# Kernel optimization log

Hardware: AMD Instinct MI355X
Metric: run time of the kernel (lower is better)

## Reference

```python
import jax, jax.numpy as jnp
import numpy as np

TOP_K = 30
NUM_RBF = 16
NUM_POS = 16
MAX_REL = 32
EDGE_FEATURES = 128
EDGE_IN = NUM_POS + NUM_RBF * 9 + 7  # 167


def _normalize(x, axis=-1):
    # torch F.normalize: x / max(||x||, 1e-12)
    return x / jnp.maximum(jnp.linalg.norm(x, axis=axis, keepdims=True), 1e-12)


def _gather_nodes(nodes, idx):
    # nodes [B,L,C], idx [B,L,K] -> [B,L,K,C]
    return jax.vmap(lambda n, i: n[i])(nodes, idx)


def _rbf(D):
    D_mu = jnp.linspace(2.0, 22.0, NUM_RBF)  # [R]
    D_sigma = (22.0 - 2.0) / NUM_RBF
    return jnp.exp(-(((D[..., None] - D_mu) / D_sigma) ** 2))


def _get_rbf(A, B, E_idx):
    # full pairwise dist then gather neighbors (faithful to source)
    D_A_B = jnp.sqrt(jnp.sum((A[:, :, None, :] - B[:, None, :, :]) ** 2, -1) + 1e-6)
    D_nb = jnp.take_along_axis(D_A_B, E_idx, axis=2)  # [B,L,K]
    return _rbf(D_nb)


def _quaternions(R):
    # R [B,L,K,3,3] -> Q [B,L,K,4]
    diag = jnp.diagonal(R, axis1=-2, axis2=-1)  # [B,L,K,3]
    Rxx, Ryy, Rzz = diag[..., 0], diag[..., 1], diag[..., 2]
    magnitudes = 0.5 * jnp.sqrt(jnp.abs(1 + jnp.stack(
        [Rxx - Ryy - Rzz, -Rxx + Ryy - Rzz, -Rxx - Ryy + Rzz], -1)))
    signs = jnp.sign(jnp.stack([
        R[..., 2, 1] - R[..., 1, 2],
        R[..., 0, 2] - R[..., 2, 0],
        R[..., 1, 0] - R[..., 0, 1]], -1))
    xyz = signs * magnitudes
    w = jnp.sqrt(jax.nn.relu(1 + jnp.sum(diag, -1, keepdims=True))) / 2.0
    return _normalize(jnp.concatenate((xyz, w), -1))


def _orientations_coarse(X, E_idx, eps=1e-6):
    B, L, _ = X.shape
    dX = X[:, 1:, :] - X[:, :-1, :]
    dX_norm = jnp.linalg.norm(dX, axis=-1)
    dX_mask = (dX_norm > 3.6) & (dX_norm < 4.0)
    dX = dX * dX_mask[:, :, None]
    U = _normalize(dX)
    u_2, u_1, u_0 = U[:, :-2, :], U[:, 1:-1, :], U[:, 2:, :]
    n_2 = _normalize(jnp.cross(u_2, u_1))
    o_1 = _normalize(u_2 - u_1)
    # local frames O [B,L-3,3,3] -> flattened, padded to [B,L,9]
    O = jnp.stack((o_1, n_2, jnp.cross(o_1, n_2)), 2).reshape(B, L - 3, 9)
    O = jnp.pad(O, ((0, 0), (1, 2), (0, 0)))
    O_neighbors = _gather_nodes(O, E_idx)        # [B,L,K,9]
    X_neighbors = _gather_nodes(X, E_idx)        # [B,L,K,3]
    O = O.reshape(B, L, 3, 3)
    O_neighbors = O_neighbors.reshape(*E_idx.shape, 3, 3)
    dXn = X_neighbors - X[:, :, None, :]
    dU = _normalize(jnp.einsum('blij,blkj->blki', O, dXn))
    R = jnp.einsum('blji,blkjm->blkim', O, O_neighbors)  # O^T @ O_nb
    Q = _quaternions(R)
    return jnp.concatenate((dU, Q), -1)  # [B,L,K,7]


def setup_inputs() -> dict:
    B, L = 2, 4096
    key = jax.random.key(0)
    ks = jax.random.split(key, 6)
    Ca = jax.random.normal(ks[0], (B, L, 3), dtype=jnp.float32)
    mask = jnp.ones((B, L), dtype=jnp.float32)
    residue_idx = jnp.arange(B * L, dtype=jnp.int32).reshape(B, L)
    chain_labels = jnp.sort(jax.random.randint(ks[1], (B, L), 0, 4), axis=-1).astype(jnp.int32)
    pos_in = 2 * MAX_REL + 1 + 1  # 66
    pos_W = jax.random.normal(ks[2], (NUM_POS, pos_in), dtype=jnp.float32) / np.sqrt(pos_in)
    pos_b = jnp.zeros((NUM_POS,), dtype=jnp.float32)
    edge_W = jax.random.normal(ks[3], (EDGE_FEATURES, EDGE_IN), dtype=jnp.float32) / np.sqrt(EDGE_IN)
    ln_g = jnp.ones((EDGE_FEATURES,), dtype=jnp.float32)
    ln_b = jnp.zeros((EDGE_FEATURES,), dtype=jnp.float32)
    return {"Ca": Ca, "mask": mask, "residue_idx": residue_idx,
            "chain_labels": chain_labels, "pos_W": pos_W, "pos_b": pos_b,
            "edge_W": edge_W, "ln_g": ln_g, "ln_b": ln_b}


def _forward(Ca, mask, residue_idx, chain_labels, pos_W, pos_b, edge_W, ln_g, ln_b):
    B, L, _ = Ca.shape
    # _dist: masked pairwise distances + kNN
    mask_2D = mask[:, :, None] * mask[:, None, :]
    dX = Ca[:, None, :, :] - Ca[:, :, None, :]
    D = mask_2D * jnp.sqrt(jnp.sum(dX ** 2, 3) + 1e-6)
    D_max = jnp.max(D, -1, keepdims=True)
    D_adjust = D + (1.0 - mask_2D) * D_max
    k = min(TOP_K, L)
    neg_vals, E_idx = jax.lax.top_k(-D_adjust, k)  # smallest-k
    D_neighbors = -neg_vals

    zeros = jnp.zeros((B, 1, 3), dtype=Ca.dtype)
    Ca_0 = jnp.concatenate([zeros, Ca[:, :-1, :]], axis=1)
    Ca_1 = Ca
    Ca_2 = jnp.concatenate([Ca[:, 1:, :], zeros], axis=1)

    O_features = _orientations_coarse(Ca, E_idx)

    RBF_all = jnp.concatenate([
        _rbf(D_neighbors),
        _get_rbf(Ca_0, Ca_0, E_idx), _get_rbf(Ca_2, Ca_2, E_idx),
        _get_rbf(Ca_0, Ca_1, E_idx), _get_rbf(Ca_0, Ca_2, E_idx),
        _get_rbf(Ca_1, Ca_0, E_idx), _get_rbf(Ca_1, Ca_2, E_idx),
        _get_rbf(Ca_2, Ca_0, E_idx), _get_rbf(Ca_2, Ca_1, E_idx)], axis=-1)

    offset = residue_idx[:, :, None] - residue_idx[:, None, :]
    offset = jnp.take_along_axis(offset, E_idx, axis=2)  # [B,L,K]
    d_chains = (chain_labels[:, :, None] - chain_labels[:, None, :] == 0).astype(jnp.int32)
    E_chains = jnp.take_along_axis(d_chains, E_idx, axis=2)

    # PositionalEncodings
    d = jnp.clip(offset + MAX_REL, 0, 2 * MAX_REL) * E_chains + (1 - E_chains) * (2 * MAX_REL + 1)
    d_onehot = jax.nn.one_hot(d, 2 * MAX_REL + 2, dtype=jnp.float32)
    E_positional = d_onehot @ pos_W.T + pos_b

    E = jnp.concatenate((E_positional, RBF_all, O_features), -1)  # [B,L,K,167]
    E = E @ edge_W.T
    mu = jnp.mean(E, -1, keepdims=True)
    var = jnp.var(E, -1, keepdims=True)
    E = (E - mu) / jnp.sqrt(var + 1e-5) * ln_g + ln_b
    return E, E_idx


def reference(Ca, mask, residue_idx, chain_labels, pos_W, pos_b, edge_W, ln_g, ln_b):
    return _forward(Ca, mask, residue_idx, chain_labels, pos_W, pos_b, edge_W, ln_g, ln_b)
```

## Files before the change

kernel.cpp:

```cpp
#include <hip/hip_runtime.h>
#include <stdint.h>

#define LL 4096
#define NB 2
#define KK 30
#define CDIM 128
#define FROW 200

typedef _Float16 half_t;
typedef half_t half8 __attribute__((ext_vector_type(8)));
typedef float f32x4 __attribute__((ext_vector_type(4)));

__device__ __forceinline__ float3 loadCa(const float* __restrict__ Ca, int b, int idx) {
    const float* p = Ca + ((size_t)(b * LL + idx)) * 3;
    return make_float3(p[0], p[1], p[2]);
}
__device__ __forceinline__ float3 shiftedCa(const float* __restrict__ Ca, int b, int idx, int sel) {
    int jj = idx + sel - 1;
    if (jj < 0 || jj >= LL) return make_float3(0.f, 0.f, 0.f);
    return loadCa(Ca, b, jj);
}
__device__ __forceinline__ float sgnf(float x) { return (x > 0.f) ? 1.f : ((x < 0.f) ? -1.f : 0.f); }
__device__ __forceinline__ float pdist(float3 a, float3 c) {
    float dx = a.x - c.x, dy = a.y - c.y, dz = a.z - c.z;
    return sqrtf(dx * dx + dy * dy + dz * dz + 1e-6f);
}

__global__ __launch_bounds__(256) void prep_kernel(const float* __restrict__ W,
                                                   const float* __restrict__ posW,
                                                   const float* __restrict__ posb,
                                                   const float* __restrict__ Ca,
                                                   half_t* __restrict__ Bp,
                                                   half_t* __restrict__ pwt,
                                                   float* __restrict__ Of) {
    int blk = blockIdx.x;
    int tid = threadIdx.x;
    if (blk < 12) {
        int idx = blk * 256 + tid;
        if (idx >= 8 * 6 * 64) return;
        int l = idx & 63;
        int ts = idx >> 6;
        int s = ts % 6, t = ts / 6;
        int n = 16 * t + (l & 15);
        int kbase = 32 * s + 8 * (l >> 4);
        half8 v;
#pragma unroll
        for (int e = 0; e < 8; e++) {
            int k = kbase + e;
            v[e] = (k < 167) ? (half_t)W[n * 167 + k] : (half_t)0.f;
        }
        *(half8*)(Bp + (size_t)idx * 8) = v;
    } else if (blk < 17) {
        int idx = (blk - 12) * 256 + tid;
        if (idx < 66 * 16) {
            int d = idx >> 4, p = idx & 15;
            pwt[d * 16 + p] = (half_t)(posW[p * 66 + d] + posb[p]);
        }
    } else {
        int t = (blk - 17) * 256 + tid;
        if (t >= NB * LL) return;
        int b = t >> 12, i = t & (LL - 1);
        float o[9] = {0.f, 0.f, 0.f, 0.f, 0.f, 0.f, 0.f, 0.f, 0.f};
        if (i >= 1 && i <= LL - 3) {
            float3 cm = loadCa(Ca, b, i - 1), cc = loadCa(Ca, b, i), cp = loadCa(Ca, b, i + 1);
            float dx0 = cc.x - cm.x, dy0 = cc.y - cm.y, dz0 = cc.z - cm.z;
            float n0 = sqrtf(dx0 * dx0 + dy0 * dy0 + dz0 * dz0);
            float k0 = (n0 > 3.6f && n0 < 4.0f) ? 1.f : 0.f;
            float s0 = k0 / fmaxf(n0 * k0, 1e-12f);
            float u2x = dx0 * s0, u2y = dy0 * s0, u2z = dz0 * s0;
            float dx1 = cp.x - cc.x, dy1 = cp.y - cc.y, dz1 = cp.z - cc.z;
            float n1 = sqrtf(dx1 * dx1 + dy1 * dy1 + dz1 * dz1);
            float k1 = (n1 > 3.6f && n1 < 4.0f) ? 1.f : 0.f;
            float s1 = k1 / fmaxf(n1 * k1, 1e-12f);
            float u1x = dx1 * s1, u1y = dy1 * s1, u1z = dz1 * s1;
            float cx = u2y * u1z - u2z * u1y;
            float cy = u2z * u1x - u2x * u1z;
            float cz = u2x * u1y - u2y * u1x;
            float cn = sqrtf(cx * cx + cy * cy + cz * cz);
            float cinv = 1.f / fmaxf(cn, 1e-12f);
            float n2x = cx * cinv, n2y = cy * cinv, n2z = cz * cinv;
            float ox = u2x - u1x, oy = u2y - u1y, oz = u2z - u1z;
            float on = sqrtf(ox * ox + oy * oy + oz * oz);
            float oinv = 1.f / fmaxf(on, 1e-12f);
            float o1x = ox * oinv, o1y = oy * oinv, o1z = oz * oinv;
            o[0] = o1x; o[1] = o1y; o[2] = o1z;
            o[3] = n2x; o[4] = n2y; o[5] = n2z;
            o[6] = o1y * n2z - o1z * n2y;
            o[7] = o1z * n2x - o1x * n2z;
            o[8] = o1x * n2y - o1y * n2x;
        }
        float* dst = Of + (size_t)t * 9;
#pragma unroll
        for (int r = 0; r < 9; r++) dst[r] = o[r];
    }
}

__global__ __launch_bounds__(256, 8) void topk_kernel(const float* __restrict__ Ca,
                                                      const float* __restrict__ mask,
                                                      int* __restrict__ eidx_ws,
                                                      float* __restrict__ dnb_ws,
                                                      float* __restrict__ out_eidx_f) {
    __shared__ unsigned long long cand[512];
    __shared__ int wint[2][4];
    __shared__ int gcnt[4];
    __shared__ float wflt[4];
    int row = blockIdx.x;
    int b = row >> 12;
    int tid = threadIdx.x;
    int w = tid >> 6, lane = tid & 63;
    float3 ci = loadCa(Ca, b, row & (LL - 1));
    float mi = mask[row];
    float dreg[16];
    float localmax = 0.f;
#pragma unroll
    for (int s = 0; s < 16; s++) {
        int j = tid + s * 256;
        const float* pj = Ca + ((size_t)(b * LL + j)) * 3;
        float dx = pj[0] - ci.x, dy = pj[1] - ci.y, dz = pj[2] - ci.z;
        float d = sqrtf(dx * dx + dy * dy + dz * dz + 1e-6f);
        float D = mi * mask[b * LL + j] * d;
        dreg[s] = D;
        localmax = fmaxf(localmax, D);
    }
#pragma unroll
    for (int o = 32; o; o >>= 1) localmax = fmaxf(localmax, __shfl_xor(localmax, o));
    if (lane == 0) wflt[w] = localmax;
    __syncthreads();
    float dmax = fmaxf(fmaxf(wflt[0], wflt[1]), fmaxf(wflt[2], wflt[3]));
    unsigned ui[16];
#pragma unroll
    for (int s = 0; s < 16; s++) {
        int j = tid + s * 256;
        float m2 = mi * mask[b * LL + j];
        ui[s] = __float_as_uint(dreg[s] + (1.0f - m2) * dmax);
    }
    unsigned lo = 0u, hi = 0x7f800000u, T = 0u;
    bool found = false;
    int p = 0;
    for (int it = 0; it < 24 && !found; ++it) {
        unsigned mid = (lo + hi) >> 1;
        int c = 0;
#pragma unroll
        for (int s = 0; s < 16; s++) c += (ui[s] < mid) ? 1 : 0;
#pragma unroll
        for (int o = 32; o; o >>= 1) c += __shfl_xor(c, o);
        if (lane == 0) wint[p][w] = c;
        __syncthreads();
        c = wint[p][0] + wint[p][1] + wint[p][2] + wint[p][3];
        p ^= 1;
        if (c < 30) lo = mid;
        else if (c > 64) hi = mid;
        else { T = mid; found = true; }
    }
    if (!found) T = hi;
    int cnt = 0;
#pragma unroll
    for (int s = 0; s < 16; s++) cnt += (ui[s] < T) ? 1 : 0;
    int inc = cnt;
#pragma unroll
    for (int o = 1; o < 64; o <<= 1) {
        int nv = __shfl_up(inc, o);
        if (lane >= o) inc += nv;
    }
    if (lane == 63) gcnt[w] = inc;
    __syncthreads();
    int C = gcnt[0] + gcnt[1] + gcnt[2] + gcnt[3];
    int waveoff = 0;
    for (int q = 0; q < 4; q++) waveoff += (q < w) ? gcnt[q] : 0;
    int slot = waveoff + inc - cnt;
#pragma unroll
    for (int s = 0; s < 16; s++) {
        if (ui[s] < T) {
            int j = tid + s * 256;
            if (slot < 512)
                cand[slot] = ((unsigned long long)ui[s] << 32) | (unsigned)j;
            slot++;
        }
    }
    __syncthreads();
    if (w != 0) return;
    if (C <= 64) {
        unsigned long long v = (lane < C) ? cand[lane] : ~0ull;
#pragma unroll
        for (int k = 2; k <= 64; k <<= 1) {
#pragma unroll
            for (int jj = k >> 1; jj > 0; jj >>= 1) {
                unsigned long long o = __shfl_xor(v, jj);
                bool take_min = (((lane & jj) == 0) == ((lane & k) == 0));
                bool lt = (o < v);
                v = (take_min == lt) ? o : v;
            }
        }
        if (lane < KK) {
            int j = (int)(v & 0xffffffffu);
            eidx_ws[row * KK + lane] = j;
            dnb_ws[row * KK + lane] = __uint_as_float((unsigned)(v >> 32));
            out_eidx_f[row * KK + lane] = (float)j;
        }
    } else {
        unsigned long long r[8];
#pragma unroll
        for (int q = 0; q < 8; q++) {
            int idx = lane + 64 * q;
            r[q] = (idx < C && idx < 512) ? cand[idx] : ~0ull;
        }
        for (int t = 0; t < KK; t++) {
            unsigned long long v = r[0];
#pragma unroll
            for (int q = 1; q < 8; q++) v = (r[q] < v) ? r[q] : v;
#pragma unroll
            for (int o = 32; o; o >>= 1) {
                unsigned long long u = __shfl_xor(v, o);
                if (u < v) v = u;
            }
            if (lane == 0) {
                int j = (int)(v & 0xffffffffu);
                eidx_ws[row * KK + t] = j;
                dnb_ws[row * KK + t] = __uint_as_float((unsigned)(v >> 32));
                out_eidx_f[row * KK + t] = (float)j;
            }
#pragma unroll
            for (int q = 0; q < 8; q++)
                if (r[q] == v) r[q] = ~0ull;
        }
    }
}

__global__ __launch_bounds__(256) void edge_kernel(const float* __restrict__ Ca,
                                                   const int* __restrict__ ridx,
                                                   const int* __restrict__ chl,
                                                   const half_t* __restrict__ pwt,
                                                   const half_t* __restrict__ Bp,
                                                   const float* __restrict__ ln_g,
                                                   const float* __restrict__ ln_b,
                                                   const float* __restrict__ Of,
                                                   const int* __restrict__ eidx_ws,
                                                   const float* __restrict__ dnb_ws,
                                                   float* __restrict__ outE) {
    __shared__ alignas(16) half_t featH[64][FROW];
    __shared__ float sD[60][10];
    __shared__ float psum[64][4];
    __shared__ float pssq[64][4];
    __shared__ float rmu[64], rinv[64];
    int row0 = blockIdx.x * 2;
    int b = row0 >> 12;
    int tid = threadIdx.x;

    if (tid < 120) {
        int e = tid >> 1, half = tid & 1;
        int isr1 = (e >= KK) ? 1 : 0;
        int grow = row0 + isr1;
        int ke = e - (isr1 ? KK : 0);
        int i = grow & (LL - 1);
        int j = eidx_ws[grow * KK + ke];
        if (half == 0) {
            float3 Pi0 = shiftedCa(Ca, b, i, 0);
            float3 Pi2 = shiftedCa(Ca, b, i, 2);
            float3 Pj0 = shiftedCa(Ca, b, j, 0);
            float3 Pj1 = loadCa(Ca, b, j);
            float3 Pj2 = shiftedCa(Ca, b, j, 2);
            sD[e][0] = dnb_ws[grow * KK + ke];
            sD[e][1] = pdist(Pi0, Pj0);
            sD[e][2] = pdist(Pi2, Pj2);
            sD[e][3] = pdist(Pi0, Pj1);
            sD[e][4] = pdist(Pi0, Pj2);
            int off = ridx[grow] - ridx[b * LL + j];
            int eqc = (chl[grow] == chl[b * LL + j]) ? 1 : 0;
            int d = off + 32;
            d = d < 0 ? 0 : (d > 64 ? 64 : d);
            d = eqc ? d : 65;
            *(half8*)&featH[e][0] = *(const half8*)(pwt + d * 16);
            *(half8*)&featH[e][8] = *(const half8*)(pwt + d * 16 + 8);
        } else {
            float3 Pi1 = loadCa(Ca, b, i);
            float3 Pi2 = shiftedCa(Ca, b, i, 2);
            float3 Pj0 = shiftedCa(Ca, b, j, 0);
            float3 Pj1 = loadCa(Ca, b, j);
            float3 Pj2 = shiftedCa(Ca, b, j, 2);
            sD[e][5] = pdist(Pi1, Pj0);
            sD[e][6] = pdist(Pi1, Pj2);
            sD[e][7] = pdist(Pi2, Pj0);
            sD[e][8] = pdist(Pi2, Pj1);
            float Oi[9], Oj[9];
#pragma unroll
            for (int r = 0; r < 9; r++) {
                Oi[r] = Of[(size_t)grow * 9 + r];
                Oj[r] = Of[((size_t)(b * LL + j)) * 9 + r];
            }
            float dx = Pj1.x - Pi1.x, dy = Pj1.y - Pi1.y, dz = Pj1.z - Pi1.z;
            float v0 = Oi[0] * dx + Oi[1] * dy + Oi[2] * dz;
            float v1 = Oi[3] * dx + Oi[4] * dy + Oi[5] * dz;
            float v2 = Oi[6] * dx + Oi[7] * dy + Oi[8] * dz;
            float nn = sqrtf(v0 * v0 + v1 * v1 + v2 * v2);
            float ninv = 1.f / fmaxf(nn, 1e-12f);
            float R[3][3];
#pragma unroll
            for (int m = 0; m < 3; m++)
#pragma unroll
                for (int n = 0; n < 3; n++)
                    R[m][n] = Oi[0 * 3 + m] * Oj[0 * 3 + n] + Oi[1 * 3 + m] * Oj[1 * 3 + n] +
                              Oi[2 * 3 + m] * Oj[2 * 3 + n];
            float Rxx = R[0][0], Ryy = R[1][1], Rzz = R[2][2];
            float m0 = 0.5f * sqrtf(fabsf(1.f + Rxx - Ryy - Rzz));
            float m1 = 0.5f * sqrtf(fabsf(1.f - Rxx + Ryy - Rzz));
            float m2 = 0.5f * sqrtf(fabsf(1.f - Rxx - Ryy + Rzz));
            float x = sgnf(R[2][1] - R[1][2]) * m0;
            float y = sgnf(R[0][2] - R[2][0]) * m1;
            float z = sgnf(R[1][0] - R[0][1]) * m2;
            float ww = 0.5f * sqrtf(fmaxf(1.f + Rxx + Ryy + Rzz, 0.f));
            float qn = sqrtf(x * x + y * y + z * z + ww * ww);
            float qi = 1.f / fmaxf(qn, 1e-12f);
            half8 h;
            h[0] = (half_t)(v0 * ninv);
            h[1] = (half_t)(v1 * ninv);
            h[2] = (half_t)(v2 * ninv);
            h[3] = (half_t)(x * qi);
            h[4] = (half_t)(y * qi);
            h[5] = (half_t)(z * qi);
            h[6] = (half_t)(ww * qi);
            h[7] = (half_t)0.f;
            half8 zv = {};
            *(half8*)&featH[e][160] = h;
            *(half8*)&featH[e][168] = zv;
            *(half8*)&featH[e][176] = zv;
            *(half8*)&featH[e][184] = zv;
        }
    } else if (tid >= 156) {
        int t = tid - 156;
        int r = 60 + t / 25, c = t % 25;
        half8 zv = {};
        *(half8*)&featH[r][c * 8] = zv;
    }
    __syncthreads();

    for (int job = tid; job < 540; job += 256) {
        int e = job / 9, q = job - e * 9;
        float D = sD[e][q];
        half8 v0, v1;
#pragma unroll
        for (int m = 0; m < 8; m++) {
            float mu = 2.0f + (4.f / 3.f) * (float)m;
            float t = (D - mu) * 0.8f;
            v0[m] = (half_t)exp2f(t * t * -1.4426950408889634f);
        }
#pragma unroll
        for (int m = 8; m < 16; m++) {
            float mu = 2.0f + (4.f / 3.f) * (float)m;
            float t = (D - mu) * 0.8f;
            v1[m - 8] = (half_t)exp2f(t * t * -1.4426950408889634f);
        }
        *(half8*)&featH[e][16 + 16 * q] = v0;
        *(half8*)&featH[e][24 + 16 * q] = v1;
    }
    __syncthreads();

    int lane = tid & 63, w = tid >> 6;
    int cc = lane & 15, g = lane >> 4;
    f32x4 zero = {0.f, 0.f, 0.f, 0.f};
    f32x4 acc[4][2];
#pragma unroll
    for (int m = 0; m < 4; m++) {
        acc[m][0] = zero;
        acc[m][1] = zero;
    }
    const half_t* b0p = Bp + ((size_t)(2 * w) * 6) * 64 * 8;
    const half_t* b1p = Bp + ((size_t)(2 * w + 1) * 6) * 64 * 8;
    for (int s = 0; s < 6; s++) {
        int ko = 32 * s + 8 * g;
        half8 af0 = *(const half8*)&featH[cc][ko];
        half8 af1 = *(const half8*)&featH[16 + cc][ko];
        half8 af2 = *(const half8*)&featH[32 + cc][ko];
        half8 af3 = *(const half8*)&featH[48 + cc][ko];
        half8 bf0 = *(const half8*)(b0p + (size_t)(s * 64 + lane) * 8);
        half8 bf1 = *(const half8*)(b1p + (size_t)(s * 64 + lane) * 8);
        acc[0][0] = __builtin_amdgcn_mfma_f32_16x16x32_f16(af0, bf0, acc[0][0], 0, 0, 0);
        acc[0][1] = __builtin_amdgcn_mfma_f32_16x16x32_f16(af0, bf1, acc[0][1], 0, 0, 0);
        acc[1][0] = __builtin_amdgcn_mfma_f32_16x16x32_f16(af1, bf0, acc[1][0], 0, 0, 0);
        acc[1][1] = __builtin_amdgcn_mfma_f32_16x16x32_f16(af1, bf1, acc[1][1], 0, 0, 0);
        acc[2][0] = __builtin_amdgcn_mfma_f32_16x16x32_f16(af2, bf0, acc[2][0], 0, 0, 0);
        acc[2][1] = __builtin_amdgcn_mfma_f32_16x16x32_f16(af2, bf1, acc[2][1], 0, 0, 0);
        acc[3][0] = __builtin_amdgcn_mfma_f32_16x16x32_f16(af3, bf0, acc[3][0], 0, 0, 0);
        acc[3][1] = __builtin_amdgcn_mfma_f32_16x16x32_f16(af3, bf1, acc[3][1], 0, 0, 0);
    }

#pragma unroll
    for (int m = 0; m < 4; m++) {
#pragma unroll
        for (int q = 0; q < 4; q++) {
            float v0 = acc[m][0][q], v1 = acc[m][1][q];
            float sp = v0 + v1;
            float qp = v0 * v0 + v1 * v1;
#pragma unroll
            for (int o = 1; o < 16; o <<= 1) {
                sp += __shfl_xor(sp, o);
                qp += __shfl_xor(qp, o);
            }
            if (cc == 0) {
                int r = 16 * m + 4 * g + q;
                psum[r][w] = sp;
                pssq[r][w] = qp;
            }
        }
    }
    __syncthreads();
    if (tid < 64) {
        float sum = psum[tid][0] + psum[tid][1] + psum[tid][2] + psum[tid][3];
        float ssq = pssq[tid][0] + pssq[tid][1] + pssq[tid][2] + pssq[tid][3];
        float mu = sum * (1.f / 128.f);
        float var = fmaxf(ssq * (1.f / 128.f) - mu * mu, 0.f);
        rmu[tid] = mu;
        rinv[tid] = 1.f / sqrtf(var + 1e-5f);
    }
    __syncthreads();

    float lgv[2], lbv[2];
#pragma unroll
    for (int tt = 0; tt < 2; tt++) {
        lgv[tt] = ln_g[32 * w + 16 * tt + cc];
        lbv[tt] = ln_b[32 * w + 16 * tt + cc];
    }
#pragma unroll
    for (int m = 0; m < 4; m++) {
#pragma unroll
        for (int q = 0; q < 4; q++) {
            int r = 16 * m + 4 * g + q;
            if (r < 60) {
                float mu = rmu[r], invs = rinv[r];
                int grow = row0 + (r >= KK ? 1 : 0);
                int ke = r - (r >= KK ? KK : 0);
                float* dst = outE + ((size_t)(grow * KK + ke)) * CDIM + 32 * w + cc;
                dst[0] = (acc[m][0][q] - mu) * invs * lgv[0] + lbv[0];
                dst[16] = (acc[m][1][q] - mu) * invs * lgv[1] + lbv[1];
            }
        }
    }
}

extern "C" void kernel_launch(void* const* d_in, const int* in_sizes, int n_in,
                              void* d_out, int out_size, void* d_ws, size_t ws_size,
                              hipStream_t stream) {
    const float* Ca = (const float*)d_in[0];
    const float* mask = (const float*)d_in[1];
    const int* ridx = (const int*)d_in[2];
    const int* chl = (const int*)d_in[3];
    const float* posW = (const float*)d_in[4];
    const float* posb = (const float*)d_in[5];
    const float* edgeW = (const float*)d_in[6];
    const float* lng = (const float*)d_in[7];
    const float* lnb = (const float*)d_in[8];

    float* outE = (float*)d_out;
    float* outEidxF = outE + (size_t)NB * LL * KK * CDIM;

    char* ws = (char*)d_ws;
    half_t* Bp = (half_t*)ws;
    half_t* pwt = (half_t*)(ws + 49152);
    float* Of = (float*)(ws + 51264);
    int* eidx = (int*)(ws + 346176);
    float* dnb = (float*)(ws + 1329216);

    prep_kernel<<<17 + (NB * LL + 255) / 256, 256, 0, stream>>>(edgeW, posW, posb, Ca, Bp, pwt, Of);
    topk_kernel<<<NB * LL, 256, 0, stream>>>(Ca, mask, eidx, dnb, outEidxF);
    edge_kernel<<<NB * LL / 2, 256, 0, stream>>>(Ca, ridx, chl, pwt, Bp, lng, lnb,
                                                 Of, eidx, dnb, outE);
}
```

Baseline: 116.3 us.

## Make top-k selection per-wave to drop block barriers, then merge wave results

Each wave now runs its own threshold binary search over its 1024 candidates with no block-level barriers per iteration. It then extracts its top-30 into shared memory, by bitonic sort when few candidates pass or by repeated argmin otherwise. Wave 0 merges the 120 per-wave candidates with 30 shuffle-reduction rounds. This removes up to 24 __syncthreads from the search loop, but adds a serial 30-round merge and, when a wave has many candidates, a costly 30-round argmin over registers. The search upper bound is also tightened to dmax, which should shorten the search.

```diff
diff --git a/kernel.cpp b/kernel.cpp
--- a/kernel.cpp
+++ b/kernel.cpp
@@ -100,9 +100,8 @@
                                                       int* __restrict__ eidx_ws,
                                                       float* __restrict__ dnb_ws,
                                                       float* __restrict__ out_eidx_f) {
-    __shared__ unsigned long long cand[512];
-    __shared__ int wint[2][4];
-    __shared__ int gcnt[4];
+    __shared__ unsigned long long wcand[4][64];
+    __shared__ unsigned long long wtop[4 * KK];
     __shared__ float wflt[4];
     int row = blockIdx.x;
     int b = row >> 12;
@@ -134,20 +133,15 @@
         float m2 = mi * mask[b * LL + j];
         ui[s] = __float_as_uint(dreg[s] + (1.0f - m2) * dmax);
     }
-    unsigned lo = 0u, hi = 0x7f800000u, T = 0u;
+    unsigned lo = 0u, hi = __float_as_uint(dmax) + 1u, T = 0u;
     bool found = false;
-    int p = 0;
-    for (int it = 0; it < 24 && !found; ++it) {
+    for (int it = 0; it < 24 && !found && (hi - lo) > 1u; ++it) {
         unsigned mid = (lo + hi) >> 1;
         int c = 0;
 #pragma unroll
         for (int s = 0; s < 16; s++) c += (ui[s] < mid) ? 1 : 0;
 #pragma unroll
         for (int o = 32; o; o >>= 1) c += __shfl_xor(c, o);
-        if (lane == 0) wint[p][w] = c;
-        __syncthreads();
-        c = wint[p][0] + wint[p][1] + wint[p][2] + wint[p][3];
-        p ^= 1;
         if (c < 30) lo = mid;
         else if (c > 64) hi = mid;
         else { T = mid; found = true; }
@@ -162,25 +156,19 @@
         int nv = __shfl_up(inc, o);
         if (lane >= o) inc += nv;
     }
-    if (lane == 63) gcnt[w] = inc;
-    __syncthreads();
-    int C = gcnt[0] + gcnt[1] + gcnt[2] + gcnt[3];
-    int waveoff = 0;
-    for (int q = 0; q < 4; q++) waveoff += (q < w) ? gcnt[q] : 0;
-    int slot = waveoff + inc - cnt;
-#pragma unroll
-    for (int s = 0; s < 16; s++) {
-        if (ui[s] < T) {
-            int j = tid + s * 256;
-            if (slot < 512)
-                cand[slot] = ((unsigned long long)ui[s] << 32) | (unsigned)j;
-            slot++;
-        }
-    }
-    __syncthreads();
-    if (w != 0) return;
+    int C = __shfl(inc, 63);
     if (C <= 64) {
-        unsigned long long v = (lane < C) ? cand[lane] : ~0ull;
+        int slot = inc - cnt;
+#pragma unroll
+        for (int s = 0; s < 16; s++) {
+            if (ui[s] < T) {
+                int j = tid + s * 256;
+                if (slot < 64)
+                    wcand[w][slot] = ((unsigned long long)ui[s] << 32) | (unsigned)j;
+                slot++;
+            }
+        }
+        unsigned long long v = (lane < C) ? wcand[w][lane] : ~0ull;
 #pragma unroll
         for (int k = 2; k <= 64; k <<= 1) {
 #pragma unroll
@@ -191,38 +179,47 @@
                 v = (take_min == lt) ? o : v;
             }
         }
-        if (lane < KK) {
-            int j = (int)(v & 0xffffffffu);
-            eidx_ws[row * KK + lane] = j;
-            dnb_ws[row * KK + lane] = __uint_as_float((unsigned)(v >> 32));
-            out_eidx_f[row * KK + lane] = (float)j;
-        }
+        if (lane < KK) wtop[w * KK + lane] = v;
     } else {
-        unsigned long long r[8];
-#pragma unroll
-        for (int q = 0; q < 8; q++) {
-            int idx = lane + 64 * q;
-            r[q] = (idx < C && idx < 512) ? cand[idx] : ~0ull;
-        }
-        for (int t = 0; t < KK; t++) {
-            unsigned long long v = r[0];
-#pragma unroll
-            for (int q = 1; q < 8; q++) v = (r[q] < v) ? r[q] : v;
+        for (int t = 0; t < KK; ++t) {
+            unsigned long long v = ~0ull;
+#pragma unroll
+            for (int s = 0; s < 16; s++) {
+                unsigned long long k = ((unsigned long long)ui[s] << 32) | (unsigned)(tid + s * 256);
+                if (k < v) v = k;
+            }
 #pragma unroll
             for (int o = 32; o; o >>= 1) {
                 unsigned long long u = __shfl_xor(v, o);
                 if (u < v) v = u;
             }
-            if (lane == 0) {
-                int j = (int)(v & 0xffffffffu);
-                eidx_ws[row * KK + t] = j;
-                dnb_ws[row * KK + t] = __uint_as_float((unsigned)(v >> 32));
-                out_eidx_f[row * KK + t] = (float)j;
-            }
-#pragma unroll
-            for (int q = 0; q < 8; q++)
-                if (r[q] == v) r[q] = ~0ull;
-        }
+#pragma unroll
+            for (int s = 0; s < 16; s++) {
+                unsigned long long k = ((unsigned long long)ui[s] << 32) | (unsigned)(tid + s * 256);
+                if (k == v) ui[s] = 0xFFFFFFFFu;
+            }
+            if (lane == 0) wtop[w * KK + t] = v;
+        }
+    }
+    __syncthreads();
+    if (w != 0) return;
+    unsigned long long r0 = (lane < 4 * KK) ? wtop[lane] : ~0ull;
+    unsigned long long r1 = (lane + 64 < 4 * KK) ? wtop[lane + 64] : ~0ull;
+    for (int t = 0; t < KK; ++t) {
+        unsigned long long v = (r0 < r1) ? r0 : r1;
+#pragma unroll
+        for (int o = 32; o; o >>= 1) {
+            unsigned long long u = __shfl_xor(v, o);
+            if (u < v) v = u;
+        }
+        if (lane == 0) {
+            int j = (int)(v & 0xffffffffu);
+            eidx_ws[row * KK + t] = j;
+            dnb_ws[row * KK + t] = __uint_as_float((unsigned)(v >> 32));
+            out_eidx_f[row * KK + t] = (float)j;
+        }
+        if (r0 == v) r0 = ~0ull;
+        if (r1 == v) r1 = ~0ull;
     }
 }
 
```

Result: slower. 145.7 us (+25.2%).
